# Optimization experiments

Measured on AMD Instinct MI355X. Metric: run time of the kernel, lower is better.

The kernel has to match this reference:

```python
import jax, jax.numpy as jnp
import numpy as np

# ---- P4M (D4) group: 8 elements, idx = 4*m + r (m: mirror bit, r: rot90 count) ----
G = 8

def _mr(i):
    return i // 4, i % 4

def _gidx(m, r):
    return 4 * (m % 2) + (r % 4)

def _comp(a, b):
    m1, r1 = _mr(a); m2, r2 = _mr(b)
    return _gidx(m1 + m2, (r1 if m2 == 0 else -r1) + r2)

_INV = [next(b for b in range(G) if _comp(a, b) == 0) for a in range(G)]
# _PERM[h, g] = index of h^{-1} * g  (left regular action on the group axis)
_PERM = np.array([[_comp(_INV[h], g) for g in range(G)] for h in range(G)])


def _spatial_transform(K, h):
    # act on the last two (spatial) kernel axes by group element h = mirror^m rot^r
    m, r = _mr(h)
    if m:
        K = jnp.flip(K, axis=-1)
    return jnp.rot90(K, k=r, axes=(-2, -1))


def _transformed_kernels(W):
    # W: [N_out, N_in, G, k, k] -> [G, N_out, N_in, G, k, k], one kernel per output group element
    return jnp.stack([_spatial_transform(W[:, :, _PERM[h]], h) for h in range(G)])


def conv_gg(x, W, padding):
    # group->group convolution. x: [B, N_in, G, H, W]; W: [N_out, N_in, G, k, k]
    B, Ni, _, H, Wd = x.shape
    No, k = W.shape[0], W.shape[-1]
    K = _transformed_kernels(W).reshape(G * No, Ni * G, k, k)
    y = jax.lax.conv_general_dilated(
        x.reshape(B, Ni * G, H, Wd), K, window_strides=(1, 1),
        padding=[(padding, padding), (padding, padding)],
        dimension_numbers=('NCHW', 'OIHW', 'NCHW'))
    Ho, Wo = y.shape[-2], y.shape[-1]
    return y.reshape(B, G, No, Ho, Wo).transpose(0, 2, 1, 3, 4)  # [B, N_out, G, Ho, Wo]


def channel_att_gg(x, W1, W2):
    # squeeze-excite over (channel, group) with group-equivariant weight sharing
    s = x.mean(axis=(-2, -1))                                  # [B, C, G]
    P1 = W1[:, :, _PERM]                                       # [M, C, G_out, G_in]
    t = jax.nn.relu(jnp.einsum('mcog,bcg->bmo', P1, s))        # [B, M, G]
    P2 = W2[:, :, _PERM]                                       # [C, M, G_out, G_in]
    return jax.nn.sigmoid(jnp.einsum('cmog,bmg->bco', P2, t))  # [B, C, G]


def spatial_att_gg(x, Wsp):
    # CBAM-style: mean/max over channels, group-equivariant 7x7 conv, sigmoid
    p = jnp.stack([x.mean(axis=1), x.max(axis=1)], axis=1)     # [B, 2, G, H, W]
    return jax.nn.sigmoid(conv_gg(p, Wsp, padding=Wsp.shape[-1] // 2))  # [B, 1, G, H, W]


def f_att_conv_gg(x, W, Wc1, Wc2, Wsp, padding):
    a_ch = channel_att_gg(x, Wc1, Wc2)[:, :, :, None, None]
    a_sp = spatial_att_gg(x, Wsp)
    return conv_gg(x * a_ch * a_sp, W, padding)


def bn3d(x, gamma, beta, eps=2e-5):
    # training-mode BatchNorm3d: stats over (B, G, H, W) per channel, biased variance
    mu = x.mean(axis=(0, 2, 3, 4), keepdims=True)
    var = ((x - mu) ** 2).mean(axis=(0, 2, 3, 4), keepdims=True)
    return (x - mu) * jax.lax.rsqrt(var + eps) * gamma[None, :, None, None, None] \
        + beta[None, :, None, None, None]


C, MID, K, SPK, B, H = 96, 48, 3, 7, 4, 56  # MID = C // ratio-reduction (ratio = C//2)


def setup_inputs() -> dict:
    key = jax.random.key(0)
    ks = jax.random.split(key, 12)
    def rn(k, shape, scale):
        return jax.random.normal(k, shape, dtype=jnp.float32) * scale
    wsc = float(np.sqrt(2.0 / (C * G * K * K)))
    asc = float(np.sqrt(2.0 / (C * G)))
    ssc = float(np.sqrt(2.0 / (2 * G * SPK * SPK)))
    return {
        'x': rn(ks[0], (B, C, G, H, H), 1.0),
        'bn1_gamma': jnp.ones((C,), jnp.float32), 'bn1_beta': jnp.zeros((C,), jnp.float32),
        'bn2_gamma': jnp.ones((C,), jnp.float32), 'bn2_beta': jnp.zeros((C,), jnp.float32),
        'c1_W': rn(ks[1], (C, C, G, K, K), wsc),
        'c1_att1': rn(ks[2], (MID, C, G), asc), 'c1_att2': rn(ks[3], (C, MID, G), asc),
        'c1_sp': rn(ks[4], (1, 2, G, SPK, SPK), ssc),
        'c2_W': rn(ks[5], (C, C, G, K, K), wsc),
        'c2_att1': rn(ks[6], (MID, C, G), asc), 'c2_att2': rn(ks[7], (C, MID, G), asc),
        'c2_sp': rn(ks[8], (1, 2, G, SPK, SPK), ssc),
    }


def reference(x, bn1_gamma, bn1_beta, bn2_gamma, bn2_beta,
              c1_W, c1_att1, c1_att2, c1_sp,
              c2_W, c2_att1, c2_att2, c2_sp):
    # fiber_map='id', stride=1 -> no group pooling, identity shortcut
    h = f_att_conv_gg(jax.nn.relu(bn3d(x, bn1_gamma, bn1_beta)),
                      c1_W, c1_att1, c1_att2, c1_sp, padding=1)
    h = f_att_conv_gg(jax.nn.relu(bn3d(h, bn2_gamma, bn2_beta)),
                      c2_W, c2_att1, c2_att2, c2_sp, padding=1)
    return x + h
```

## Files before the change

### kernel.cpp

```cpp
#include <hip/hip_runtime.h>
#include <math.h>

#define NG 8
#define C96 96
#define NMID 48
#define HW 56
#define PIX 3136
#define GHW 25088
#define CIN 768
#define NPIXT 9633792
#define BN_N 100352
#define PADW 58
#define PADPIX 3364
#define WTK 589824
#define PPL 3968

typedef __attribute__((ext_vector_type(8))) short bf16x8;
typedef __attribute__((ext_vector_type(4))) float f32x4;

__device__ __forceinline__ int d_comp(int a, int b){
  int m1=a>>2, r1=a&3, m2=b>>2, r2=b&3;
  int m=(m1+m2)&1;
  int r = (m2==0) ? (r1+r2) : (r2-r1);
  r = (r+4)&3;
  return 4*m+r;
}
__device__ __forceinline__ int d_inv(int a){ return (a>>2) ? a : ((4-(a&3))&3); }
__device__ __forceinline__ int d_perm(int h, int g){ return d_comp(d_inv(h), g); }

__device__ __forceinline__ void d_src(int h, int dy, int dx, int n, int* sy, int* sx){
  int r=h&3, m=h>>2, e=n-1;
  int y,x;
  if(r==0){y=dy; x=dx;}
  else if(r==1){y=dx; x=e-dy;}
  else if(r==2){y=e-dy; x=e-dx;}
  else {y=e-dx; x=dy;}
  if(m) x = e-x;
  *sy=y; *sx=x;
}

__device__ __forceinline__ unsigned short f2bf(float f){
  unsigned int u = __builtin_bit_cast(unsigned int, f);
  unsigned int r = (u + 0x7FFFu + ((u>>16)&1u)) >> 16;
  return (unsigned short)r;
}

__device__ __forceinline__ void gload_lds16(const void* g, void* l){
  __builtin_amdgcn_global_load_lds((const __attribute__((address_space(1))) unsigned int*)g,
                                   (__attribute__((address_space(3))) unsigned int*)l, 16, 0, 0);
}

#define VMCNT6() do { asm volatile("s_waitcnt vmcnt(6)" ::: "memory"); \
                      __builtin_amdgcn_sched_barrier(0); } while(0)
#define VMCNT2() do { asm volatile("s_waitcnt vmcnt(2)" ::: "memory"); \
                      __builtin_amdgcn_sched_barrier(0); } while(0)
#define VMCNT0() do { asm volatile("s_waitcnt vmcnt(0)" ::: "memory"); \
                      __builtin_amdgcn_sched_barrier(0); } while(0)
#define BAR() do { __builtin_amdgcn_s_barrier(); __builtin_amdgcn_sched_barrier(0); } while(0)

__global__ void k_bn_stats(const float* __restrict__ in, float* __restrict__ spart){
  __shared__ float sm[8];
  int c = blockIdx.x, s = blockIdx.y;
  int b = s>>1, half = s&1;
  const float4* p = (const float4*)(in + ((size_t)(b*C96 + c))*GHW) + half*(GHW/8);
  float sum=0.f, sum2=0.f;
  for (int i=threadIdx.x; i<GHW/8; i+=256){
    float4 v = p[i];
    sum  += v.x+v.y+v.z+v.w;
    sum2 += v.x*v.x+v.y*v.y+v.z*v.z+v.w*v.w;
  }
  #pragma unroll
  for (int off=32; off>0; off>>=1){ sum += __shfl_down(sum,off); sum2 += __shfl_down(sum2,off); }
  int lane=threadIdx.x&63, wid=threadIdx.x>>6;
  if(lane==0){ sm[wid]=sum; sm[4+wid]=sum2; }
  __syncthreads();
  if(threadIdx.x==0){
    float a=sm[0]+sm[1]+sm[2]+sm[3], b2=sm[4]+sm[5]+sm[6]+sm[7];
    spart[(c*8+s)*2]   = a;
    spart[(c*8+s)*2+1] = b2;
  }
}

__global__ __launch_bounds__(256) void k_pool(const float* __restrict__ in,
    const float* __restrict__ spart, const float* __restrict__ gamma, const float* __restrict__ beta,
    float* __restrict__ pp){
  __shared__ float scs[C96], shs[C96];
  int tid = threadIdx.x;
  if (tid < C96){
    float s=0.f, s2=0.f;
    #pragma unroll
    for (int k=0;k<8;k++){ s += spart[(tid*8+k)*2]; s2 += spart[(tid*8+k)*2+1]; }
    float mean = s*(1.f/BN_N);
    float var  = s2*(1.f/BN_N) - mean*mean;
    float sc = gamma[tid]*rsqrtf(var + 2e-5f);
    scs[tid] = sc; shs[tid] = beta[tid] - mean*sc;
  }
  __syncthreads();
  int bg = blockIdx.y; int b = bg>>3, g = bg&7;
  int px = blockIdx.x*256 + tid;
  if (px >= PIX) return;
  float pm = 0.f, pmx = 0.f;
  for (int c = 0; c < C96; c++){
    size_t idx = ((size_t)((b*C96 + c)*8 + g))*PIX + px;
    float v = fmaxf(fmaf(in[idx], scs[c], shs[c]), 0.f);
    pm += v; pmx = fmaxf(pmx, v);
  }
  int y = px/HW, x = px - y*HW;
  pp[(size_t)(b*16 + g)*PPL     + (y+3)*64 + (x+3)] = pm;
  pp[(size_t)(b*16 + 8 + g)*PPL + (y+3)*64 + (x+3)] = pmx;
}

__global__ void k_chan(const float* __restrict__ in, const float* __restrict__ spart,
    const float* __restrict__ gamma, const float* __restrict__ beta, float* __restrict__ sout){
  int bcg = blockIdx.x;
  int c = (bcg >> 3) % C96;
  float s=0.f, s2=0.f;
  #pragma unroll
  for (int k=0;k<8;k++){ s += spart[(c*8+k)*2]; s2 += spart[(c*8+k)*2+1]; }
  float mean = s*(1.f/BN_N);
  float var  = s2*(1.f/BN_N) - mean*mean;
  float sc = gamma[c]*rsqrtf(var + 2e-5f);
  float sh = beta[c] - mean*sc;
  const float4* p = (const float4*)(in + (size_t)bcg*PIX);
  float acc=0.f;
  for (int i=threadIdx.x; i<PIX/4; i+=64){
    float4 v = p[i];
    acc += fmaxf(fmaf(v.x,sc,sh),0.f) + fmaxf(fmaf(v.y,sc,sh),0.f)
         + fmaxf(fmaf(v.z,sc,sh),0.f) + fmaxf(fmaf(v.w,sc,sh),0.f);
  }
  #pragma unroll
  for(int off=32;off>0;off>>=1) acc += __shfl_down(acc,off);
  if(threadIdx.x==0) sout[bcg] = acc * (1.f/3136.f);
}

__global__ void k_ca(const float* __restrict__ sbuf, const float* __restrict__ W1,
                     const float* __restrict__ W2, float* __restrict__ ach){
  __shared__ float sl[CIN], tl[NMID*8];
  int b = blockIdx.x, tid = threadIdx.x;
  sl[tid] = sbuf[b*CIN + tid];
  __syncthreads();
  int o = tid & 7;
  int pg[8];
  #pragma unroll
  for (int g=0; g<8; g++) pg[g] = d_perm(o, g);
  if (tid < NMID*8){
    int m = tid >> 3;
    float acc = 0.f;
    for (int c=0; c<C96; c++){
      #pragma unroll
      for (int g=0; g<8; g++) acc += W1[(m*C96+c)*8+pg[g]] * sl[c*8+g];
    }
    tl[tid] = fmaxf(acc, 0.f);
  }
  __syncthreads();
  {
    int c = tid >> 3;
    float acc = 0.f;
    for (int m=0; m<NMID; m++){
      #pragma unroll
      for (int g=0; g<8; g++) acc += W2[(c*NMID+m)*8+pg[g]] * tl[(m<<3)+g];
    }
    ach[b*CIN + tid] = 1.f/(1.f+__expf(-acc));
  }
}

__global__ __launch_bounds__(256) void k_sp_conv(const float* __restrict__ pp,
    const float* __restrict__ Wsp, float* __restrict__ aspt){
  __shared__ float wl[2*8*49];
  int bh = blockIdx.y; int b=bh>>3, h=bh&7;
  for(int idx=threadIdx.x; idx<784; idx+=256){
    int i = idx/392; int rem = idx-i*392;
    int g = rem/49; int kk = rem-g*49;
    int dy=kk/7, dx=kk-dy*7;
    int pg = d_perm(h,g);
    int sy,sx; d_src(h,dy,dx,7,&sy,&sx);
    wl[idx] = Wsp[(i*8+pg)*49 + sy*7+sx] * (i==0 ? (1.f/96.f) : 1.f);
  }
  __syncthreads();
  int pix = blockIdx.x*256 + threadIdx.x;
  if(pix>=PIX) return;
  int y=pix/HW, x=pix-y*HW;
  const float* base = pp + (size_t)(b*16)*PPL + y*64 + x;
  float acc=0.f;
  for(int ig=0; ig<16; ig++){
    const float* pb = base + (size_t)ig*PPL;
    const float* wb = wl + ig*49;
    #pragma unroll
    for(int dy=0; dy<7; dy++){
      #pragma unroll
      for(int dx=0; dx<7; dx++)
        acc = fmaf(pb[dy*64+dx], wb[dy*7+dx], acc);
    }
  }
  aspt[((size_t)b*PIX + pix)*8 + h] = 1.f/(1.f+__expf(-acc));
}

__global__ void k_zerob(uint4* __restrict__ xp, uint4* __restrict__ pp){
  uint4 z = (uint4){0u,0u,0u,0u};
  int i = blockIdx.x*256 + threadIdx.x;
  if (blockIdx.x < 248){ pp[i] = z; return; }
  int r = i - 63488;
  if (r >= 87552) return;
  int b = r / 21888;
  int q = r - b*21888;
  int p = q / 96, j = q - p*96;
  int y, x;
  if (p < 58){ y=0; x=p; }
  else if (p < 116){ y=57; x=p-58; }
  else if (p < 172){ y=p-115; x=0; }
  else { y=p-171; x=57; }
  xp[(size_t)(b*PADPIX + y*PADW + x)*96 + j] = z;
}

__global__ __launch_bounds__(256) void k_mod_t(const float* __restrict__ in,
    const float* __restrict__ spart, const float* __restrict__ gamma, const float* __restrict__ beta,
    const float* __restrict__ ach, const float* __restrict__ aspt,
    unsigned int* __restrict__ XpU){
  __shared__ float tile[64][65];
  __shared__ float scs8[8], shs8[8];
  int b = blockIdx.z;
  int cg0 = blockIdx.y*64;
  int pix0 = blockIdx.x*64;
  int tid = threadIdx.x;
  if (tid < 8){
    int c = (cg0>>3) + tid;
    float s=0.f, s2=0.f;
    #pragma unroll
    for (int k=0;k<8;k++){ s += spart[(c*8+k)*2]; s2 += spart[(c*8+k)*2+1]; }
    float mean = s*(1.f/BN_N);
    float var  = s2*(1.f/BN_N) - mean*mean;
    float sc = gamma[c]*rsqrtf(var + 2e-5f);
    scs8[tid] = sc; shs8[tid] = beta[c] - mean*sc;
  }
  __syncthreads();
  int lane = tid & 63, w = tid >> 6;
  for (int r = w; r < 64; r += 4){
    int cg = cg0 + r;
    float a1 = ach[b*CIN + cg];
    float raw = in[(size_t)(b*CIN + cg)*PIX + pix0 + lane];
    float v = fmaxf(fmaf(raw, scs8[r>>3], shs8[r>>3]), 0.f);
    tile[r][lane] = v * a1;
  }
  __syncthreads();
  int half = lane >> 5;
  int cgA = (lane & 31)*2;
  #pragma unroll
  for (int it = 0; it < 8; it++){
    int p = it*8 + w*2 + half;
    int pix = pix0 + p;
    int y = pix/HW, x = pix - y*HW;
    float2 a2 = *(const float2*)(aspt + ((size_t)b*PIX + pix)*8 + (cgA&7));
    float vA = tile[cgA][p]   * a2.x;
    float vB = tile[cgA+1][p] * a2.y;
    unsigned int u = (unsigned int)f2bf(vA) | ((unsigned int)f2bf(vB) << 16);
    XpU[(((size_t)b*PADPIX + (y+1)*PADW + (x+1))*CIN + cg0 + cgA) >> 1] = u;
  }
}

__global__ void k_ktb2(const float* __restrict__ W1src, const float* __restrict__ W2src,
                       unsigned short* __restrict__ Wt1, unsigned short* __restrict__ Wt2){
  const float* W = blockIdx.y ? W2src : W1src;
  unsigned short* Wt = blockIdx.y ? Wt2 : Wt1;
  int idx = blockIdx.x*256 + threadIdx.x;
  int ci = idx % CIN;
  int t2 = idx / CIN;
  int co = t2 % CIN;
  int kk = t2 / CIN;
  int h = co/C96, o = co - h*C96;
  int i = ci >> 3, g = ci & 7;
  int dy = kk/3, dx = kk - dy*3;
  int sy, sx; d_src(h, dy, dx, 3, &sy, &sx);
  float v = W[((o*C96 + i)*8 + d_perm(h,g))*9 + sy*3 + sx];
  Wt[idx] = f2bf(v);
}

__global__ __launch_bounds__(256, 3) void k_convmf(const unsigned short* __restrict__ Xp,
    const unsigned short* __restrict__ Wt, const float* __restrict__ resid,
    float* __restrict__ out){
  __shared__ unsigned short lds[24576];
  char* ldsb = (char*)lds;
  int tid = threadIdx.x, lane = tid & 63, w = tid >> 6;
  int col = lane & 15, kg = lane >> 4;

  int bid = blockIdx.x;
  int wgid = (bid & 7)*84 + (bid >> 3);
  int m = wgid/112; int rem = wgid - m*112;
  int b = rem/28;  int rp = rem - b*28;
  int y0 = rp*2, co0 = m*128;

  int xgo[4], xds[4];
  #pragma unroll
  for (int t = 0; t < 4; t++){
    int slot = t*256 + tid;
    int row = slot >> 8;
    int px  = (slot >> 2) & 63;
    int g   = slot & 3;
    int sg  = g ^ ((px >> 1) & 3);
    xgo[t] = (b*PADPIX + (y0+row)*PADW + px)*CIN + sg*8;
    xds[t] = slot*16;
  }
  int wgo[2], wds[2];
  #pragma unroll
  for (int j = 0; j < 2; j++){
    int r  = w*32 + j*16 + (lane>>2);
    int sg = (lane&3) ^ ((lane>>3)&3);
    wgo[j] = (co0 + r)*CIN + sg*8;
    wds[j] = 32768 + r*64 + (lane&3)*16;
  }
  int awo[2];
  #pragma unroll
  for (int mf = 0; mf < 2; mf++){
    int r = w*32 + mf*16 + col;
    awo[mf] = 32768 + r*64 + ((kg ^ ((col>>1)&3)) << 4);
  }
  int bb[3][7];
  #pragma unroll
  for (int nf=0; nf<7; nf++){
    int q2 = nf*16 + col;
    int qyl = (q2 >= 56) ? 1 : 0;
    int qx = q2 - 56*qyl;
    #pragma unroll
    for (int dx=0; dx<3; dx++){
      int px = qx + dx;
      bb[dx][nf] = qyl*4096 + px*64 + ((kg ^ ((px>>1)&3)) << 4);
    }
  }

  f32x4 acc[2][7];
  #pragma unroll
  for (int mf=0; mf<2; mf++)
    #pragma unroll
    for (int nf=0; nf<7; nf++)
      acc[mf][nf] = (f32x4){0.f,0.f,0.f,0.f};

  #pragma unroll
  for (int j = 0; j < 2; j++) gload_lds16(Wt + wgo[j], ldsb + wds[j]);
  #pragma unroll
  for (int t = 0; t < 4; t++) gload_lds16(Xp + xgo[t], ldsb + xds[t]);
  VMCNT0();
  BAR();

  int q = 0;
  for (int chunk = 0; chunk < 23; chunk++){
    const int xb = (chunk & 1) * 16384;
    #pragma unroll
    for (int kk = 0; kk < 9; kk++){
      {
        int kk2 = (kk == 8) ? 0 : kk+1;
        int c2  = (kk == 8) ? chunk+1 : chunk;
        size_t gofs = (size_t)kk2*WTK + (c2 << 5);
        int dofs = (q^1)*8192;
        gload_lds16(Wt + gofs + wgo[0], ldsb + dofs + wds[0]);
        gload_lds16(Wt + gofs + wgo[1], ldsb + dofs + wds[1]);
      }
      if (kk == 6){
        #pragma unroll
        for (int t = 0; t < 4; t++)
          gload_lds16(Xp + xgo[t] + (chunk+1)*32, ldsb + (xb^16384) + xds[t]);
      }
      if (kk == 6 || kk == 7) VMCNT6();
      else                    VMCNT2();
      const int wq = q*8192;
      bf16x8 A0 = *(const bf16x8*)(ldsb + awo[0] + wq);
      bf16x8 A1 = *(const bf16x8*)(ldsb + awo[1] + wq);
      const int dyk = kk/3, dxk = kk - dyk*3;
      const int dofs2 = xb + dyk*4096;
      __builtin_amdgcn_s_setprio(1);
      #pragma unroll
      for (int nf = 0; nf < 7; nf++){
        bf16x8 B = *(const bf16x8*)(ldsb + bb[dxk][nf] + dofs2);
        acc[0][nf] = __builtin_amdgcn_mfma_f32_16x16x32_bf16(A0, B, acc[0][nf], 0,0,0);
        acc[1][nf] = __builtin_amdgcn_mfma_f32_16x16x32_bf16(A1, B, acc[1][nf], 0,0,0);
      }
      __builtin_amdgcn_s_setprio(0);
      q ^= 1;
    }
    BAR();
  }
  {
    const int xb = (23 & 1) * 16384;
    #pragma unroll
    for (int kk = 0; kk < 9; kk++){
      if (kk < 8){
        size_t gofs = (size_t)(kk+1)*WTK + (23 << 5);
        int dofs = (q^1)*8192;
        gload_lds16(Wt + gofs + wgo[0], ldsb + dofs + wds[0]);
        gload_lds16(Wt + gofs + wgo[1], ldsb + dofs + wds[1]);
        VMCNT2();
      } else {
        VMCNT0();
      }
      const int wq = q*8192;
      bf16x8 A0 = *(const bf16x8*)(ldsb + awo[0] + wq);
      bf16x8 A1 = *(const bf16x8*)(ldsb + awo[1] + wq);
      const int dyk = kk/3, dxk = kk - dyk*3;
      const int dofs2 = xb + dyk*4096;
      __builtin_amdgcn_s_setprio(1);
      #pragma unroll
      for (int nf = 0; nf < 7; nf++){
        bf16x8 B = *(const bf16x8*)(ldsb + bb[dxk][nf] + dofs2);
        acc[0][nf] = __builtin_amdgcn_mfma_f32_16x16x32_bf16(A0, B, acc[0][nf], 0,0,0);
        acc[1][nf] = __builtin_amdgcn_mfma_f32_16x16x32_bf16(A1, B, acc[1][nf], 0,0,0);
      }
      __builtin_amdgcn_s_setprio(0);
      q ^= 1;
    }
  }

  #pragma unroll
  for (int mf = 0; mf < 2; mf++){
    int co_b = co0 + w*32 + mf*16;
    int h = co_b/C96;
    int ob = co_b - h*C96 + kg*4;
    #pragma unroll
    for (int nf = 0; nf < 7; nf++){
      int qq = nf*16 + col;
      #pragma unroll
      for (int r = 0; r < 4; r++){
        size_t oi = ((size_t)((b*C96 + ob + r)*8 + h))*PIX + y0*56 + qq;
        float v = acc[mf][nf][r];
        if (resid) v += resid[oi];
        out[oi] = v;
      }
    }
  }
}

static void run_layer(const float* bn_in,
                      const float* a1W, const float* a2W, const float* spW,
                      const float* bng, const float* bnb,
                      const float* resid, float* convout,
                      float* spart, float* sbuf, float* ach, float* ppP, float* aspt,
                      unsigned short* Wt, unsigned short* Xp, hipStream_t stream)
{
  k_bn_stats<<<dim3(C96,8),256,0,stream>>>(bn_in, spart);
  k_pool<<<dim3(13,32),256,0,stream>>>(bn_in, spart, bng, bnb, ppP);
  k_chan<<<4*C96*NG,64,0,stream>>>(bn_in, spart, bng, bnb, sbuf);
  k_ca<<<4,CIN,0,stream>>>(sbuf, a1W, a2W, ach);
  k_sp_conv<<<dim3(13,32),256,0,stream>>>(ppP, spW, aspt);
  k_mod_t<<<dim3(PIX/64, CIN/64, 4),256,0,stream>>>(bn_in, spart, bng, bnb, ach, aspt, (unsigned int*)Xp);
  k_convmf<<<672,256,0,stream>>>(Xp, Wt, resid, convout);
}

extern "C" void kernel_launch(void* const* d_in, const int* in_sizes, int n_in,
                              void* d_out, int out_size, void* d_ws, size_t ws_size,
                              hipStream_t stream) {
  const float* x    = (const float*)d_in[0];
  const float* bn1g = (const float*)d_in[1];
  const float* bn1b = (const float*)d_in[2];
  const float* bn2g = (const float*)d_in[3];
  const float* bn2b = (const float*)d_in[4];
  const float* c1W  = (const float*)d_in[5];
  const float* c1a1 = (const float*)d_in[6];
  const float* c1a2 = (const float*)d_in[7];
  const float* c1sp = (const float*)d_in[8];
  const float* c2W  = (const float*)d_in[9];
  const float* c2a1 = (const float*)d_in[10];
  const float* c2a2 = (const float*)d_in[11];
  const float* c2sp = (const float*)d_in[12];
  float* out = (float*)d_out;
  float* ws  = (float*)d_ws;

  float* bufA = ws;
  unsigned short* Wt1 = (unsigned short*)(bufA + NPIXT);
  unsigned short* Wt2 = Wt1 + 9*CIN*CIN;
  unsigned short* Xp  = Wt2 + 9*CIN*CIN;
  float* spart = (float*)(Xp + (size_t)4*PADPIX*CIN);
  float* sbuf  = spart + 1536;
  float* ach   = sbuf + 4*C96*NG;
  float* ppP   = ach + 4*C96*NG;
  float* aspt  = ppP + 4*16*PPL;

  k_ktb2<<<dim3((9*CIN*CIN)/256, 2),256,0,stream>>>(c1W, c2W, Wt1, Wt2);
  k_zerob<<<590,256,0,stream>>>((uint4*)Xp, (uint4*)ppP);

  run_layer(x, c1a1, c1a2, c1sp, bn1g, bn1b, nullptr, bufA,
            spart, sbuf, ach, ppP, aspt, Wt1, Xp, stream);
  run_layer(bufA, c2a1, c2a2, c2sp, bn2g, bn2b, x, out,
            spart, sbuf, ach, ppP, aspt, Wt2, Xp, stream);
}
```

Measured before the change: 544.2 us.

## Halve conv block to two waves with 64-row output tiles; add ILP accumulators

The main MFMA conv kernel now runs 128 threads per block instead of 256, so each wave computes a 64x112 output tile (four M fragments) rather than 32x112. Each B fragment read from LDS is therefore reused across four MFMAs, cutting LDS traffic per MFMA, and the per-thread global-to-LDS load counts and vmcnt waits are scaled up to match. The cost is more accumulator registers, a lower occupancy target (launch bounds 128,2), and fewer waves to hide latency. Several small kernels (pool, channel attention, spatial conv) also gain split accumulators to break serial FMA dependency chains.

```diff
diff --git a/kernel.cpp b/kernel.cpp
--- a/kernel.cpp
+++ b/kernel.cpp
@@ -50,9 +50,9 @@
                                    (__attribute__((address_space(3))) unsigned int*)l, 16, 0, 0);
 }
 
-#define VMCNT6() do { asm volatile("s_waitcnt vmcnt(6)" ::: "memory"); \
-                      __builtin_amdgcn_sched_barrier(0); } while(0)
-#define VMCNT2() do { asm volatile("s_waitcnt vmcnt(2)" ::: "memory"); \
+#define VMCNT12() do { asm volatile("s_waitcnt vmcnt(12)" ::: "memory"); \
+                       __builtin_amdgcn_sched_barrier(0); } while(0)
+#define VMCNT4() do { asm volatile("s_waitcnt vmcnt(4)" ::: "memory"); \
                       __builtin_amdgcn_sched_barrier(0); } while(0)
 #define VMCNT0() do { asm volatile("s_waitcnt vmcnt(0)" ::: "memory"); \
                       __builtin_amdgcn_sched_barrier(0); } while(0)
@@ -99,15 +99,18 @@
   int bg = blockIdx.y; int b = bg>>3, g = bg&7;
   int px = blockIdx.x*256 + tid;
   if (px >= PIX) return;
-  float pm = 0.f, pmx = 0.f;
-  for (int c = 0; c < C96; c++){
-    size_t idx = ((size_t)((b*C96 + c)*8 + g))*PIX + px;
-    float v = fmaxf(fmaf(in[idx], scs[c], shs[c]), 0.f);
-    pm += v; pmx = fmaxf(pmx, v);
+  float pm0=0.f, pm1=0.f, mx0=0.f, mx1=0.f;
+  for (int c = 0; c < C96; c += 2){
+    size_t i0 = ((size_t)((b*C96 + c)*8 + g))*PIX + px;
+    size_t i1 = i0 + (size_t)8*PIX;
+    float v0 = fmaxf(fmaf(in[i0], scs[c],   shs[c]),   0.f);
+    float v1 = fmaxf(fmaf(in[i1], scs[c+1], shs[c+1]), 0.f);
+    pm0 += v0; mx0 = fmaxf(mx0, v0);
+    pm1 += v1; mx1 = fmaxf(mx1, v1);
   }
   int y = px/HW, x = px - y*HW;
-  pp[(size_t)(b*16 + g)*PPL     + (y+3)*64 + (x+3)] = pm;
-  pp[(size_t)(b*16 + 8 + g)*PPL + (y+3)*64 + (x+3)] = pmx;
+  pp[(size_t)(b*16 + g)*PPL     + (y+3)*64 + (x+3)] = pm0+pm1;
+  pp[(size_t)(b*16 + 8 + g)*PPL + (y+3)*64 + (x+3)] = fmaxf(mx0,mx1);
 }
 
 __global__ void k_chan(const float* __restrict__ in, const float* __restrict__ spart,
@@ -145,22 +148,26 @@
   for (int g=0; g<8; g++) pg[g] = d_perm(o, g);
   if (tid < NMID*8){
     int m = tid >> 3;
-    float acc = 0.f;
-    for (int c=0; c<C96; c++){
-      #pragma unroll
-      for (int g=0; g<8; g++) acc += W1[(m*C96+c)*8+pg[g]] * sl[c*8+g];
-    }
-    tl[tid] = fmaxf(acc, 0.f);
+    float a0 = 0.f, a1 = 0.f;
+    for (int c=0; c<C96; c+=2){
+      #pragma unroll
+      for (int g=0; g<8; g++) a0 += W1[(m*C96+c)*8+pg[g]] * sl[c*8+g];
+      #pragma unroll
+      for (int g=0; g<8; g++) a1 += W1[(m*C96+c+1)*8+pg[g]] * sl[(c+1)*8+g];
+    }
+    tl[tid] = fmaxf(a0+a1, 0.f);
   }
   __syncthreads();
   {
     int c = tid >> 3;
-    float acc = 0.f;
-    for (int m=0; m<NMID; m++){
-      #pragma unroll
-      for (int g=0; g<8; g++) acc += W2[(c*NMID+m)*8+pg[g]] * tl[(m<<3)+g];
-    }
-    ach[b*CIN + tid] = 1.f/(1.f+__expf(-acc));
+    float a0 = 0.f, a1 = 0.f;
+    for (int m=0; m<NMID; m+=2){
+      #pragma unroll
+      for (int g=0; g<8; g++) a0 += W2[(c*NMID+m)*8+pg[g]] * tl[(m<<3)+g];
+      #pragma unroll
+      for (int g=0; g<8; g++) a1 += W2[(c*NMID+m+1)*8+pg[g]] * tl[((m+1)<<3)+g];
+    }
+    ach[b*CIN + tid] = 1.f/(1.f+__expf(-(a0+a1)));
   }
 }
 
@@ -181,7 +188,8 @@
   if(pix>=PIX) return;
   int y=pix/HW, x=pix-y*HW;
   const float* base = pp + (size_t)(b*16)*PPL + y*64 + x;
-  float acc=0.f;
+  float ac[4] = {0.f,0.f,0.f,0.f};
+  #pragma unroll
   for(int ig=0; ig<16; ig++){
     const float* pb = base + (size_t)ig*PPL;
     const float* wb = wl + ig*49;
@@ -189,9 +197,10 @@
     for(int dy=0; dy<7; dy++){
       #pragma unroll
       for(int dx=0; dx<7; dx++)
-        acc = fmaf(pb[dy*64+dx], wb[dy*7+dx], acc);
-    }
-  }
+        ac[ig&3] = fmaf(pb[dy*64+dx], wb[dy*7+dx], ac[ig&3]);
+    }
+  }
+  float acc = (ac[0]+ac[1]) + (ac[2]+ac[3]);
   aspt[((size_t)b*PIX + pix)*8 + h] = 1.f/(1.f+__expf(-acc));
 }
 
@@ -274,7 +283,7 @@
   Wt[idx] = f2bf(v);
 }
 
-__global__ __launch_bounds__(256, 3) void k_convmf(const unsigned short* __restrict__ Xp,
+__global__ __launch_bounds__(128, 2) void k_convmf(const unsigned short* __restrict__ Xp,
     const unsigned short* __restrict__ Wt, const float* __restrict__ resid,
     float* __restrict__ out){
   __shared__ unsigned short lds[24576];
@@ -288,10 +297,10 @@
   int b = rem/28;  int rp = rem - b*28;
   int y0 = rp*2, co0 = m*128;
 
-  int xgo[4], xds[4];
-  #pragma unroll
-  for (int t = 0; t < 4; t++){
-    int slot = t*256 + tid;
+  int xgo[8], xds[8];
+  #pragma unroll
+  for (int t = 0; t < 8; t++){
+    int slot = t*128 + tid;
     int row = slot >> 8;
     int px  = (slot >> 2) & 63;
     int g   = slot & 3;
@@ -299,18 +308,18 @@
     xgo[t] = (b*PADPIX + (y0+row)*PADW + px)*CIN + sg*8;
     xds[t] = slot*16;
   }
-  int wgo[2], wds[2];
-  #pragma unroll
-  for (int j = 0; j < 2; j++){
-    int r  = w*32 + j*16 + (lane>>2);
+  int wgo[4], wds[4];
+  #pragma unroll
+  for (int j = 0; j < 4; j++){
+    int r  = w*64 + j*16 + (lane>>2);
     int sg = (lane&3) ^ ((lane>>3)&3);
     wgo[j] = (co0 + r)*CIN + sg*8;
     wds[j] = 32768 + r*64 + (lane&3)*16;
   }
-  int awo[2];
-  #pragma unroll
-  for (int mf = 0; mf < 2; mf++){
-    int r = w*32 + mf*16 + col;
+  int awo[4];
+  #pragma unroll
+  for (int mf = 0; mf < 4; mf++){
+    int r = w*64 + mf*16 + col;
     awo[mf] = 32768 + r*64 + ((kg ^ ((col>>1)&3)) << 4);
   }
   int bb[3][7];
@@ -326,17 +335,17 @@
     }
   }
 
-  f32x4 acc[2][7];
-  #pragma unroll
-  for (int mf=0; mf<2; mf++)
+  f32x4 acc[4][7];
+  #pragma unroll
+  for (int mf=0; mf<4; mf++)
     #pragma unroll
     for (int nf=0; nf<7; nf++)
       acc[mf][nf] = (f32x4){0.f,0.f,0.f,0.f};
 
   #pragma unroll
-  for (int j = 0; j < 2; j++) gload_lds16(Wt + wgo[j], ldsb + wds[j]);
-  #pragma unroll
-  for (int t = 0; t < 4; t++) gload_lds16(Xp + xgo[t], ldsb + xds[t]);
+  for (int j = 0; j < 4; j++) gload_lds16(Wt + wgo[j], ldsb + wds[j]);
+  #pragma unroll
+  for (int t = 0; t < 8; t++) gload_lds16(Xp + xgo[t], ldsb + xds[t]);
   VMCNT0();
   BAR();
 
@@ -350,19 +359,22 @@
         int c2  = (kk == 8) ? chunk+1 : chunk;
         size_t gofs = (size_t)kk2*WTK + (c2 << 5);
         int dofs = (q^1)*8192;
-        gload_lds16(Wt + gofs + wgo[0], ldsb + dofs + wds[0]);
-        gload_lds16(Wt + gofs + wgo[1], ldsb + dofs + wds[1]);
+        #pragma unroll
+        for (int j = 0; j < 4; j++)
+          gload_lds16(Wt + gofs + wgo[j], ldsb + dofs + wds[j]);
       }
       if (kk == 6){
         #pragma unroll
-        for (int t = 0; t < 4; t++)
+        for (int t = 0; t < 8; t++)
           gload_lds16(Xp + xgo[t] + (chunk+1)*32, ldsb + (xb^16384) + xds[t]);
       }
-      if (kk == 6 || kk == 7) VMCNT6();
-      else                    VMCNT2();
+      if (kk == 6 || kk == 7) VMCNT12();
+      else                    VMCNT4();
       const int wq = q*8192;
       bf16x8 A0 = *(const bf16x8*)(ldsb + awo[0] + wq);
       bf16x8 A1 = *(const bf16x8*)(ldsb + awo[1] + wq);
+      bf16x8 A2 = *(const bf16x8*)(ldsb + awo[2] + wq);
+      bf16x8 A3 = *(const bf16x8*)(ldsb + awo[3] + wq);
       const int dyk = kk/3, dxk = kk - dyk*3;
       const int dofs2 = xb + dyk*4096;
       __builtin_amdgcn_s_setprio(1);
@@ -371,6 +383,8 @@
         bf16x8 B = *(const bf16x8*)(ldsb + bb[dxk][nf] + dofs2);
         acc[0][nf] = __builtin_amdgcn_mfma_f32_16x16x32_bf16(A0, B, acc[0][nf], 0,0,0);
         acc[1][nf] = __builtin_amdgcn_mfma_f32_16x16x32_bf16(A1, B, acc[1][nf], 0,0,0);
+        acc[2][nf] = __builtin_amdgcn_mfma_f32_16x16x32_bf16(A2, B, acc[2][nf], 0,0,0);
+        acc[3][nf] = __builtin_amdgcn_mfma_f32_16x16x32_bf16(A3, B, acc[3][nf], 0,0,0);
       }
       __builtin_amdgcn_s_setprio(0);
       q ^= 1;
@@ -378,21 +392,24 @@
     BAR();
   }
   {
-    const int xb = (23 & 1) * 16384;
+    const int xb = 16384;
     #pragma unroll
     for (int kk = 0; kk < 9; kk++){
       if (kk < 8){
         size_t gofs = (size_t)(kk+1)*WTK + (23 << 5);
         int dofs = (q^1)*8192;
-        gload_lds16(Wt + gofs + wgo[0], ldsb + dofs + wds[0]);
-        gload_lds16(Wt + gofs + wgo[1], ldsb + dofs + wds[1]);
-        VMCNT2();
+        #pragma unroll
+        for (int j = 0; j < 4; j++)
+          gload_lds16(Wt + gofs + wgo[j], ldsb + dofs + wds[j]);
+        VMCNT4();
       } else {
         VMCNT0();
       }
       const int wq = q*8192;
       bf16x8 A0 = *(const bf16x8*)(ldsb + awo[0] + wq);
       bf16x8 A1 = *(const bf16x8*)(ldsb + awo[1] + wq);
+      bf16x8 A2 = *(const bf16x8*)(ldsb + awo[2] + wq);
+      bf16x8 A3 = *(const bf16x8*)(ldsb + awo[3] + wq);
       const int dyk = kk/3, dxk = kk - dyk*3;
       const int dofs2 = xb + dyk*4096;
       __builtin_amdgcn_s_setprio(1);
@@ -401,6 +418,8 @@
         bf16x8 B = *(const bf16x8*)(ldsb + bb[dxk][nf] + dofs2);
         acc[0][nf] = __builtin_amdgcn_mfma_f32_16x16x32_bf16(A0, B, acc[0][nf], 0,0,0);
         acc[1][nf] = __builtin_amdgcn_mfma_f32_16x16x32_bf16(A1, B, acc[1][nf], 0,0,0);
+        acc[2][nf] = __builtin_amdgcn_mfma_f32_16x16x32_bf16(A2, B, acc[2][nf], 0,0,0);
+        acc[3][nf] = __builtin_amdgcn_mfma_f32_16x16x32_bf16(A3, B, acc[3][nf], 0,0,0);
       }
       __builtin_amdgcn_s_setprio(0);
       q ^= 1;
@@ -408,8 +427,8 @@
   }
 
   #pragma unroll
-  for (int mf = 0; mf < 2; mf++){
-    int co_b = co0 + w*32 + mf*16;
+  for (int mf = 0; mf < 4; mf++){
+    int co_b = co0 + w*64 + mf*16;
     int h = co_b/C96;
     int ob = co_b - h*C96 + kg*4;
     #pragma unroll
@@ -439,7 +458,7 @@
   k_ca<<<4,CIN,0,stream>>>(sbuf, a1W, a2W, ach);
   k_sp_conv<<<dim3(13,32),256,0,stream>>>(ppP, spW, aspt);
   k_mod_t<<<dim3(PIX/64, CIN/64, 4),256,0,stream>>>(bn_in, spart, bng, bnb, ach, aspt, (unsigned int*)Xp);
-  k_convmf<<<672,256,0,stream>>>(Xp, Wt, resid, convout);
+  k_convmf<<<672,128,0,stream>>>(Xp, Wt, resid, convout);
 }
 
 extern "C" void kernel_launch(void* const* d_in, const int* in_sizes, int n_in,
```

New measurement: 486.0 us. 10.7% less time.
